# Kernel tuning notes

Measured on AMD Instinct MI355X. Metric: run time of the kernel, lower is better.

The kernel has to match this reference:

```python
import jax, jax.numpy as jnp
import numpy as np

H = 10           # lstm_hidden / attn_hidden
OUT = 2          # output_size
VTH = 0.5        # args.vth (LSNN threshold, beta=0 so fixed)
DT = 1e-3
TAU_SYN_INV = 1.0 / 5e-3
TAU_MEM_INV = 1.0 / 1e-2


def _bn(x, g, b, eps=1e-5):
    # TdBatchNorm1d in ANN mode: BatchNorm1d over channel dim of (B, C, T), batch stats
    m = x.mean(axis=(0, 2), keepdims=True)
    v = x.var(axis=(0, 2), keepdims=True)
    return g[None, :, None] * (x - m) * jax.lax.rsqrt(v + eps) + b[None, :, None]


def _lin(x, W):
    # ModuleLayer(Linear): apply linear over channel dim of (B, C, T)
    return jnp.einsum('bct,hc->bht', x, W)


def setup_inputs() -> dict:
    key = jax.random.key(0)
    ks = jax.random.split(key, 12)
    B, C, T = 32, 64, 1024
    f32 = jnp.float32
    ones = jnp.ones((H,), f32)
    zeros = jnp.zeros((H,), f32)
    def n(k, shape, s=0.3):
        return jax.random.normal(k, shape, f32) * s
    return {
        'bs1': jax.random.normal(ks[0], (B, 1), f32),
        'bs2': jax.random.normal(ks[1], (B, 1), f32),
        'beeg': jax.random.normal(ks[2], (B, C, T), f32),
        'targets': jax.random.randint(ks[3], (B,), 0, 2),
        'W_ef': n(ks[4], (H, C)), 'b_ef': jnp.zeros((H,), f32),
        'g_i': ones, 'be_i': zeros,
        'Wq': n(ks[5], (H, H)), 'g_q': ones, 'be_q': zeros,
        'Wk': n(ks[6], (H, H)), 'g_k': ones, 'be_k': zeros,
        'Wv': n(ks[7], (H, H)), 'g_v': ones, 'be_v': zeros,
        'Wc': n(ks[8], (H, H)), 'g_c': ones, 'be_c': zeros,
        'W_in': n(ks[9], (H, H)), 'W_rec': n(ks[10], (H, H)),
        'W_cls': n(ks[11], (OUT, H)), 'b_cls': jnp.zeros((OUT,), f32),
    }


def _forward(beeg, W_ef, b_ef, g_i, be_i, Wq, g_q, be_q, Wk, g_k, be_k,
             Wv, g_v, be_v, Wc, g_c, be_c, W_in, W_rec, W_cls, b_cls):
    # front embedding + BNi + tanh : (B, C, T) -> (B, H, T)
    x = jnp.tanh(_bn(_lin(beeg, W_ef) + b_ef[None, :, None], g_i, be_i))
    # self-attention (need_sa, full dot_product path)
    q = jax.nn.relu(_bn(_lin(x, Wq), g_q, be_q))
    k = jax.nn.relu(_bn(_lin(x, Wk), g_k, be_k))
    v = jnp.tanh(_bn(_lin(x, Wv), g_v, be_v))
    w = jnp.einsum('bht,bhs->bts', q, k) / H              # (B, T, T)
    av = jnp.einsum('bts,bhs->bht', w, v)                  # (B, H, T)
    x = jax.nn.relu(_bn(_lin(av, Wc), g_c, be_c))
    # LSNN recurrence over time (norse-style LSNN, beta=0, b fixed at VTH)
    xs = jnp.transpose(x, (2, 0, 1))                       # (T, B, H)
    B = xs.shape[1]
    dtype = xs.dtype
    def lsnn_step(state, xt):
        z, vm, cur, b = state
        i_jump = cur + xt @ W_in.T + z @ W_rec.T
        v_dec = vm + DT * TAU_MEM_INV * (i_jump - vm)
        i_dec = i_jump * (1.0 - DT * TAU_SYN_INV)
        z_new = (v_dec > b).astype(dtype)
        v_new = (1.0 - z_new) * v_dec
        return (z_new, v_new, i_dec, b), z_new
    z0 = jnp.zeros((B, H), dtype)
    init = (z0, z0, z0, jnp.full((B, H), VTH, dtype))
    _, zs = jax.lax.scan(lsnn_step, init, xs)              # (T, B, H) spikes
    # LILinearCell classifier, stepped over time, then mean over T
    def li_step(state, zt):
        vm, cur = state
        i_new = cur * (1.0 - DT * TAU_SYN_INV) + zt @ W_cls.T + b_cls
        v_new = vm * (1.0 - DT * TAU_MEM_INV) + DT * TAU_MEM_INV * i_new
        return (v_new, i_new), v_new
    s0 = jnp.zeros((B, OUT), dtype)
    _, vs = jax.lax.scan(li_step, (s0, s0), zs)            # (T, B, 2)
    return vs.mean(axis=0)                                 # (B, 2) = sum/step


def reference(bs1, bs2, beeg, targets, W_ef, b_ef, g_i, be_i, Wq, g_q, be_q,
              Wk, g_k, be_k, Wv, g_v, be_v, Wc, g_c, be_c, W_in, W_rec,
              W_cls, b_cls):
    out = _forward(beeg, W_ef, b_ef, g_i, be_i, Wq, g_q, be_q, Wk, g_k, be_k,
                   Wv, g_v, be_v, Wc, g_c, be_c, W_in, W_rec, W_cls, b_cls)
    return out
```

## Files before the change

### kernel.cpp

```cpp
#include <hip/hip_runtime.h>
#include <math.h>


constexpr int B = 32, C = 64, T = 1024, H = 10;
constexpr int NT = 1024;
constexpr int RS = 1028;

struct Params {
  const float *beeg, *W_ef, *b_ef, *g_i, *be_i, *Wq, *g_q, *be_q, *Wk, *g_k,
      *be_k, *Wv, *g_v, *be_v, *Wc, *g_c, *be_c, *W_in, *W_rec, *W_cls, *b_cls;
  int* cnt;
  double *P1, *P2, *P3;
  float* out;
};

template <int CTRL>
__device__ inline float dadd(float v) {
  int x = __builtin_amdgcn_update_dpp(0, __float_as_int(v), CTRL, 0xf, 0xf,
                                      true);
  return v + __int_as_float(x);
}
__device__ inline float wred63(float v) {
  v = dadd<0x111>(v);
  v = dadd<0x112>(v);
  v = dadd<0x114>(v);
  v = dadd<0x118>(v);
  v = dadd<0x142>(v);
  v = dadd<0x143>(v);
  return v;
}

__device__ inline float ftanh(float x) {
  float e = __builtin_amdgcn_exp2f(x * 2.8853900817779268f);
  float r = __builtin_amdgcn_rcpf(e + 1.0f);
  return fmaf(-2.0f, r, 1.0f);
}

__device__ inline void gbar(int* cnt, int phase, int tid) {
  __syncthreads();
  if (tid == 0) {
    __hip_atomic_fetch_add(&cnt[phase], 1, __ATOMIC_RELEASE,
                           __HIP_MEMORY_SCOPE_AGENT);
    while (__hip_atomic_load(&cnt[phase], __ATOMIC_RELAXED,
                             __HIP_MEMORY_SCOPE_AGENT) < B)
      __builtin_amdgcn_s_sleep(2);
  }
  __syncthreads();
}

__global__ void __launch_bounds__(NT) fused19(Params p) {
  const int b = blockIdx.x, tid = threadIdx.x;
  const int lane = tid & 63, wid = tid >> 6;

  __shared__ __align__(16) float slab[T * 11];
  __shared__ __align__(16) float gtab[T];
  __shared__ double dred2[60 * 17 + 4];
  __shared__ double dtot[60];
  __shared__ float stM[30], stI[30], Ms[100], Nl[100];
  __shared__ float kxl[NT * 11];

  float* swred = slab;
  float* mpw   = slab + 1024;

  {
    const float L2A = -0.15200309344504995f;
    const float L2D = -0.32192809488736235f;
    float m0 = (float)(T - tid);
    gtab[tid] = (9.0f * (1.0f - exp2f(m0 * L2A)) -
                 4.0f * (1.0f - exp2f(m0 * L2D))) * (1.0f / (float)T);
  }

  auto combine = [&](double* P, int Q2) {
    for (int id = tid; id < Q2 * 16; id += NT) {
      int ch = id >> 4, i = id & 15;
      double s = __hip_atomic_load(&P[ch * 32 + i], __ATOMIC_RELAXED,
                                   __HIP_MEMORY_SCOPE_AGENT) +
                 __hip_atomic_load(&P[ch * 32 + 16 + i], __ATOMIC_RELAXED,
                                   __HIP_MEMORY_SCOPE_AGENT);
      dred2[ch * 17 + i] = s;
    }
    __syncthreads();
    if (tid < Q2) {
      double s = 0.0;
#pragma unroll
      for (int i = 0; i < 16; ++i) s += dred2[tid * 17 + i];
      dtot[tid] = s;
    }
    __syncthreads();
  };

  float p1[H];
#pragma unroll
  for (int h = 0; h < H; ++h) p1[h] = p.b_ef[h];
  {
    const float* bp = p.beeg + (size_t)b * C * T;
#pragma unroll 8
    for (int c = 0; c < C; ++c) {
      float v = bp[(size_t)c * T + tid];
#pragma unroll
      for (int h = 0; h < H; ++h)
        p1[h] = fmaf(v, p.W_ef[h * C + c], p1[h]);
    }
  }
#pragma unroll
  for (int h = 0; h < H; ++h) {
    float r1 = wred63(p1[h]);
    float r2 = wred63(p1[h] * p1[h]);
    if (lane == 63) { swred[wid * 60 + h] = r1; swred[wid * 60 + 10 + h] = r2; }
  }
  __syncthreads();
  if (tid < 20) {
    float s = 0.f;
#pragma unroll
    for (int w = 0; w < 16; ++w) s += swred[w * 60 + tid];
    __hip_atomic_store(&p.P1[tid * 32 + b], (double)s, __ATOMIC_RELAXED,
                       __HIP_MEMORY_SCOPE_AGENT);
  }
  gbar(p.cnt, 0, tid);
  combine(p.P1, 20);
  if (tid < 10) {
    double mean = dtot[tid] * (1.0 / 32768.0);
    double var  = dtot[10 + tid] * (1.0 / 32768.0) - mean * mean;
    stM[tid] = (float)mean;
    stI[tid] = (float)(1.0 / sqrt(var + 1e-5));
  }
  __syncthreads();

  float xa[H];
#pragma unroll
  for (int j = 0; j < H; ++j)
    xa[j] = ftanh(p.g_i[j] * (p1[j] - stM[j]) * stI[j] + p.be_i[j]);
#pragma unroll
  for (int h = 0; h < H; ++h) {
    float qa = 0.f, ka = 0.f, va = 0.f;
#pragma unroll
    for (int j = 0; j < H; ++j) {
      qa = fmaf(xa[j], p.Wq[h * H + j], qa);
      ka = fmaf(xa[j], p.Wk[h * H + j], ka);
      va = fmaf(xa[j], p.Wv[h * H + j], va);
    }
    float r1 = wred63(qa), r2 = wred63(qa * qa);
    float r3 = wred63(ka), r4 = wred63(ka * ka);
    float r5 = wred63(va), r6 = wred63(va * va);
    if (lane == 63) {
      swred[wid * 60 + h]      = r1; swred[wid * 60 + 30 + h] = r2;
      swred[wid * 60 + 10 + h] = r3; swred[wid * 60 + 40 + h] = r4;
      swred[wid * 60 + 20 + h] = r5; swred[wid * 60 + 50 + h] = r6;
    }
  }
  __syncthreads();
  if (tid < 60) {
    float s = 0.f;
#pragma unroll
    for (int w = 0; w < 16; ++w) s += swred[w * 60 + tid];
    __hip_atomic_store(&p.P2[tid * 32 + b], (double)s, __ATOMIC_RELAXED,
                       __HIP_MEMORY_SCOPE_AGENT);
  }
  gbar(p.cnt, 1, tid);
  combine(p.P2, 60);
  if (tid < 30) {
    double mean = dtot[tid] * (1.0 / 32768.0);
    double var  = dtot[30 + tid] * (1.0 / 32768.0) - mean * mean;
    stM[tid] = (float)mean;
    stI[tid] = (float)(1.0 / sqrt(var + 1e-5));
  }
  __syncthreads();

  {
    float vx[H];
#pragma unroll
    for (int h = 0; h < H; ++h) {
      float ka = 0.f, va = 0.f;
#pragma unroll
      for (int j = 0; j < H; ++j) {
        ka = fmaf(xa[j], p.Wk[h * H + j], ka);
        va = fmaf(xa[j], p.Wv[h * H + j], va);
      }
      kxl[tid * 11 + h] =
          fmaxf(p.g_k[h] * (ka - stM[10 + h]) * stI[10 + h] + p.be_k[h], 0.f);
      vx[h] = ftanh(p.g_v[h] * (va - stM[20 + h]) * stI[20 + h] + p.be_v[h]);
    }
#pragma unroll 1
    for (int i = 0; i < H; ++i) {
      float ki = kxl[tid * 11 + i];
#pragma unroll
      for (int j = 0; j < H; ++j) {
        float r = wred63(ki * vx[j]);
        if (lane == 63) mpw[wid * 100 + i * 10 + j] = r;
      }
    }
  }
  __syncthreads();
  if (tid < 100) {
    float s = 0.f;
#pragma unroll
    for (int w = 0; w < 16; ++w) s += mpw[w * 100 + tid];
    Ms[tid] = s;
  }
  __syncthreads();

  if (tid < 100) {
    int i = tid / 10, h = tid % 10;
    float a = 0.f;
#pragma unroll
    for (int j = 0; j < H; ++j) a = fmaf(Ms[i * 10 + j], p.Wc[h * H + j], a);
    Nl[tid] = a * 0.1f;
  }
  __syncthreads();
  float pca[H];
  {
    float qv[H];
#pragma unroll
    for (int h = 0; h < H; ++h) {
      float qa = 0.f;
#pragma unroll
      for (int j = 0; j < H; ++j) qa = fmaf(xa[j], p.Wq[h * H + j], qa);
      qv[h] = fmaxf(p.g_q[h] * (qa - stM[h]) * stI[h] + p.be_q[h], 0.f);
    }
#pragma unroll
    for (int h = 0; h < H; ++h) {
      float a = 0.f;
#pragma unroll
      for (int i = 0; i < H; ++i) a = fmaf(qv[i], Nl[i * 10 + h], a);
      pca[h] = a;
    }
  }
#pragma unroll
  for (int h = 0; h < H; ++h) {
    float r1 = wred63(pca[h]);
    float r2 = wred63(pca[h] * pca[h]);
    if (lane == 63) { swred[wid * 60 + h] = r1; swred[wid * 60 + 10 + h] = r2; }
  }
  __syncthreads();
  if (tid < 20) {
    float s = 0.f;
#pragma unroll
    for (int w = 0; w < 16; ++w) s += swred[w * 60 + tid];
    __hip_atomic_store(&p.P3[tid * 32 + b], (double)s, __ATOMIC_RELAXED,
                       __HIP_MEMORY_SCOPE_AGENT);
  }
  gbar(p.cnt, 2, tid);
  combine(p.P3, 20);
  if (tid < 10) {
    double mean = dtot[tid] * (1.0 / 32768.0);
    double var  = dtot[10 + tid] * (1.0 / 32768.0) - mean * mean;
    stM[tid] = (float)mean;
    stI[tid] = (float)(1.0 / sqrt(var + 1e-5));
  }
  __syncthreads();

  {
    float ca[H];
#pragma unroll
    for (int j = 0; j < H; ++j)
      ca[j] = fmaxf(p.g_c[j] * (pca[j] - stM[j]) * stI[j] + p.be_c[j], 0.f);
#pragma unroll
    for (int h = 0; h < H; ++h) {
      float a = 0.f;
#pragma unroll
      for (int j = 0; j < H; ++j) a = fmaf(ca[j], p.W_in[h * H + j], a);
      slab[h * RS + tid] = a;
    }
  }
  __syncthreads();

  if (tid < 64) {
    const float gtot = 4.9365234375f;

    const int slot = lane < H ? lane : 0;
    const float* row = slab + slot * RS;
    float wrf[H];
#pragma unroll
    for (int j = 0; j < H; ++j)
      wrf[j] = (lane < H) ? p.W_rec[lane * H + j] : 0.f;

    float accp = 0.f, vm = 0.f, S = 0.f;
    float zf = 0.f;

    auto step = [&](float iin, float gt) {
      float zj[H];
#pragma unroll
      for (int j = 0; j < H; ++j)
        zj[j] = __int_as_float(
            __builtin_amdgcn_readlane(__float_as_int(zf), j));
      float acc0 = fmaf(0.8f, accp, iin);
      float acc1 = 0.f;
#pragma unroll
      for (int j = 0; j < H; j += 2) {
        acc0 = fmaf(zj[j],     wrf[j],     acc0);
        acc1 = fmaf(zj[j + 1], wrf[j + 1], acc1);
      }
      float acc = acc0 + acc1;
      float v_dec = fmaf(0.1f, acc - vm, vm);
      bool z = v_dec > 0.5f;
      vm = z ? 0.f : v_dec;
      zf = z ? 1.0f : 0.0f;
      S = fmaf(zf, gt, S);
      accp = acc;
    };

    float4 iA = *(const float4*)&row[0];
    float4 iB = *(const float4*)&row[4];
    float4 gA = *(const float4*)&gtab[0], gB = *(const float4*)&gtab[4];

    for (int t8 = 0; t8 < T - 8; t8 += 8) {
      float4 iN1 = *(const float4*)&row[t8 + 8];
      float4 iN2 = *(const float4*)&row[t8 + 12];
      float4 gN1 = *(const float4*)&gtab[t8 + 8];
      float4 gN2 = *(const float4*)&gtab[t8 + 12];
      step(iA.x, gA.x); step(iA.y, gA.y); step(iA.z, gA.z); step(iA.w, gA.w);
      step(iB.x, gB.x); step(iB.y, gB.y); step(iB.z, gB.z); step(iB.w, gB.w);
      iA = iN1; iB = iN2; gA = gN1; gB = gN2;
    }
    step(iA.x, gA.x); step(iA.y, gA.y); step(iA.z, gA.z); step(iA.w, gA.w);
    step(iB.x, gB.x); step(iB.y, gB.y); step(iB.z, gB.z); step(iB.w, gB.w);

    int li = lane < H ? lane : 0;
    float c0 = (lane < H) ? S * p.W_cls[li]     : 0.f;
    float c1 = (lane < H) ? S * p.W_cls[H + li] : 0.f;
    float r0 = wred63(c0), r1 = wred63(c1);
    if (lane == 63) {
      p.out[b * 2 + 0] = r0 + gtot * p.b_cls[0];
      p.out[b * 2 + 1] = r1 + gtot * p.b_cls[1];
    }
  }
}

extern "C" void kernel_launch(void* const* d_in, const int* in_sizes, int n_in,
                              void* d_out, int out_size, void* d_ws, size_t ws_size,
                              hipStream_t stream) {
  Params p;
  p.beeg  = (const float*)d_in[2];
  p.W_ef  = (const float*)d_in[4];
  p.b_ef  = (const float*)d_in[5];
  p.g_i   = (const float*)d_in[6];
  p.be_i  = (const float*)d_in[7];
  p.Wq    = (const float*)d_in[8];
  p.g_q   = (const float*)d_in[9];
  p.be_q  = (const float*)d_in[10];
  p.Wk    = (const float*)d_in[11];
  p.g_k   = (const float*)d_in[12];
  p.be_k  = (const float*)d_in[13];
  p.Wv    = (const float*)d_in[14];
  p.g_v   = (const float*)d_in[15];
  p.be_v  = (const float*)d_in[16];
  p.Wc    = (const float*)d_in[17];
  p.g_c   = (const float*)d_in[18];
  p.be_c  = (const float*)d_in[19];
  p.W_in  = (const float*)d_in[20];
  p.W_rec = (const float*)d_in[21];
  p.W_cls = (const float*)d_in[22];
  p.b_cls = (const float*)d_in[23];

  char* ws = (char*)d_ws;
  p.cnt = (int*)ws;
  p.P1  = (double*)(ws + 256);
  p.P2  = (double*)(ws + 256 + 5120);
  p.P3  = (double*)(ws + 256 + 5120 + 15360);
  p.out = (float*)d_out;

  (void)hipMemsetAsync(d_ws, 0, 256, stream);
  fused19<<<dim3(B), dim3(NT), 0, stream>>>(p);
}
```

Baseline: 221.9 us.

## Halve block size and process two timesteps per thread with packed FMA

Reduces the block from 1024 to 512 threads, with each thread handling timesteps t and t+512. The per-thread math uses two-wide float vectors so the compiler can emit packed FMA instructions. The two halves are summed before each wave reduction, so cross-wave reduction work halves. The kxl scratch buffer is dropped in favour of a transposed layout reusing the slab, which needs an extra barrier. The costs are more registers per thread and less thread-level parallelism during the serial-heavy phases.

```diff
diff --git a/kernel.cpp b/kernel.cpp
--- a/kernel.cpp
+++ b/kernel.cpp
@@ -3,8 +3,14 @@
 
 
 constexpr int B = 32, C = 64, T = 1024, H = 10;
-constexpr int NT = 1024;
+constexpr int NT = 512;
 constexpr int RS = 1028;
+
+using v2f = float __attribute__((ext_vector_type(2)));
+__device__ inline v2f v2(float s) { v2f r; r.x = s; r.y = s; return r; }
+__device__ inline v2f vfma(v2f a, v2f b, v2f c) {
+  return __builtin_elementwise_fma(a, b, c);
+}
 
 struct Params {
   const float *beeg, *W_ef, *b_ef, *g_i, *be_i, *Wq, *g_q, *be_q, *Wk, *g_k,
@@ -48,26 +54,29 @@
   __syncthreads();
 }
 
-__global__ void __launch_bounds__(NT) fused19(Params p) {
+__global__ void __launch_bounds__(NT) fused21(Params p) {
   const int b = blockIdx.x, tid = threadIdx.x;
   const int lane = tid & 63, wid = tid >> 6;
+  const int t0 = tid, t1 = tid + NT;
 
   __shared__ __align__(16) float slab[T * 11];
   __shared__ __align__(16) float gtab[T];
   __shared__ double dred2[60 * 17 + 4];
   __shared__ double dtot[60];
   __shared__ float stM[30], stI[30], Ms[100], Nl[100];
-  __shared__ float kxl[NT * 11];
 
   float* swred = slab;
-  float* mpw   = slab + 1024;
+  float* kxt   = slab;
+  float* mpw   = slab + 10240;
 
   {
     const float L2A = -0.15200309344504995f;
     const float L2D = -0.32192809488736235f;
-    float m0 = (float)(T - tid);
-    gtab[tid] = (9.0f * (1.0f - exp2f(m0 * L2A)) -
-                 4.0f * (1.0f - exp2f(m0 * L2D))) * (1.0f / (float)T);
+    float m0 = (float)(T - t0), m1 = (float)(T - t1);
+    gtab[t0] = (9.0f * (1.0f - exp2f(m0 * L2A)) -
+                4.0f * (1.0f - exp2f(m0 * L2D))) * (1.0f / (float)T);
+    gtab[t1] = (9.0f * (1.0f - exp2f(m1 * L2A)) -
+                4.0f * (1.0f - exp2f(m1 * L2D))) * (1.0f / (float)T);
   }
 
   auto combine = [&](double* P, int Q2) {
@@ -89,30 +98,32 @@
     __syncthreads();
   };
 
-  float p1[H];
-#pragma unroll
-  for (int h = 0; h < H; ++h) p1[h] = p.b_ef[h];
+  v2f p1[H];
+#pragma unroll
+  for (int h = 0; h < H; ++h) p1[h] = v2(p.b_ef[h]);
   {
     const float* bp = p.beeg + (size_t)b * C * T;
 #pragma unroll 8
     for (int c = 0; c < C; ++c) {
-      float v = bp[(size_t)c * T + tid];
+      v2f vab;
+      vab.x = bp[(size_t)c * T + t0];
+      vab.y = bp[(size_t)c * T + t1];
 #pragma unroll
       for (int h = 0; h < H; ++h)
-        p1[h] = fmaf(v, p.W_ef[h * C + c], p1[h]);
+        p1[h] = vfma(vab, v2(p.W_ef[h * C + c]), p1[h]);
     }
   }
 #pragma unroll
   for (int h = 0; h < H; ++h) {
-    float r1 = wred63(p1[h]);
-    float r2 = wred63(p1[h] * p1[h]);
+    float r1 = wred63(p1[h].x + p1[h].y);
+    float r2 = wred63(p1[h].x * p1[h].x + p1[h].y * p1[h].y);
     if (lane == 63) { swred[wid * 60 + h] = r1; swred[wid * 60 + 10 + h] = r2; }
   }
   __syncthreads();
   if (tid < 20) {
     float s = 0.f;
 #pragma unroll
-    for (int w = 0; w < 16; ++w) s += swred[w * 60 + tid];
+    for (int w = 0; w < 8; ++w) s += swred[w * 60 + tid];
     __hip_atomic_store(&p.P1[tid * 32 + b], (double)s, __ATOMIC_RELAXED,
                        __HIP_MEMORY_SCOPE_AGENT);
   }
@@ -126,22 +137,24 @@
   }
   __syncthreads();
 
-  float xa[H];
-#pragma unroll
-  for (int j = 0; j < H; ++j)
-    xa[j] = ftanh(p.g_i[j] * (p1[j] - stM[j]) * stI[j] + p.be_i[j]);
+  v2f xv[H];
+#pragma unroll
+  for (int j = 0; j < H; ++j) {
+    xv[j].x = ftanh(p.g_i[j] * (p1[j].x - stM[j]) * stI[j] + p.be_i[j]);
+    xv[j].y = ftanh(p.g_i[j] * (p1[j].y - stM[j]) * stI[j] + p.be_i[j]);
+  }
 #pragma unroll
   for (int h = 0; h < H; ++h) {
-    float qa = 0.f, ka = 0.f, va = 0.f;
+    v2f q = v2(0.f), k = v2(0.f), v = v2(0.f);
 #pragma unroll
     for (int j = 0; j < H; ++j) {
-      qa = fmaf(xa[j], p.Wq[h * H + j], qa);
-      ka = fmaf(xa[j], p.Wk[h * H + j], ka);
-      va = fmaf(xa[j], p.Wv[h * H + j], va);
-    }
-    float r1 = wred63(qa), r2 = wred63(qa * qa);
-    float r3 = wred63(ka), r4 = wred63(ka * ka);
-    float r5 = wred63(va), r6 = wred63(va * va);
+      q = vfma(xv[j], v2(p.Wq[h * H + j]), q);
+      k = vfma(xv[j], v2(p.Wk[h * H + j]), k);
+      v = vfma(xv[j], v2(p.Wv[h * H + j]), v);
+    }
+    float r1 = wred63(q.x + q.y), r2 = wred63(q.x * q.x + q.y * q.y);
+    float r3 = wred63(k.x + k.y), r4 = wred63(k.x * k.x + k.y * k.y);
+    float r5 = wred63(v.x + v.y), r6 = wred63(v.x * v.x + v.y * v.y);
     if (lane == 63) {
       swred[wid * 60 + h]      = r1; swred[wid * 60 + 30 + h] = r2;
       swred[wid * 60 + 10 + h] = r3; swred[wid * 60 + 40 + h] = r4;
@@ -152,7 +165,7 @@
   if (tid < 60) {
     float s = 0.f;
 #pragma unroll
-    for (int w = 0; w < 16; ++w) s += swred[w * 60 + tid];
+    for (int w = 0; w < 8; ++w) s += swred[w * 60 + tid];
     __hip_atomic_store(&p.P2[tid * 32 + b], (double)s, __ATOMIC_RELAXED,
                        __HIP_MEMORY_SCOPE_AGENT);
   }
@@ -167,25 +180,30 @@
   __syncthreads();
 
   {
-    float vx[H];
+    v2f vx[H];
 #pragma unroll
     for (int h = 0; h < H; ++h) {
-      float ka = 0.f, va = 0.f;
+      v2f k = v2(0.f), v = v2(0.f);
 #pragma unroll
       for (int j = 0; j < H; ++j) {
-        ka = fmaf(xa[j], p.Wk[h * H + j], ka);
-        va = fmaf(xa[j], p.Wv[h * H + j], va);
+        k = vfma(xv[j], v2(p.Wk[h * H + j]), k);
+        v = vfma(xv[j], v2(p.Wv[h * H + j]), v);
       }
-      kxl[tid * 11 + h] =
-          fmaxf(p.g_k[h] * (ka - stM[10 + h]) * stI[10 + h] + p.be_k[h], 0.f);
-      vx[h] = ftanh(p.g_v[h] * (va - stM[20 + h]) * stI[20 + h] + p.be_v[h]);
-    }
+      kxt[h * NT + tid] =
+          fmaxf(p.g_k[h] * (k.x - stM[10 + h]) * stI[10 + h] + p.be_k[h], 0.f);
+      kxt[(H + h) * NT + tid] =
+          fmaxf(p.g_k[h] * (k.y - stM[10 + h]) * stI[10 + h] + p.be_k[h], 0.f);
+      vx[h].x = ftanh(p.g_v[h] * (v.x - stM[20 + h]) * stI[20 + h] + p.be_v[h]);
+      vx[h].y = ftanh(p.g_v[h] * (v.y - stM[20 + h]) * stI[20 + h] + p.be_v[h]);
+    }
+    __syncthreads();
 #pragma unroll 1
     for (int i = 0; i < H; ++i) {
-      float ki = kxl[tid * 11 + i];
+      float kia = kxt[i * NT + tid];
+      float kib = kxt[(H + i) * NT + tid];
 #pragma unroll
       for (int j = 0; j < H; ++j) {
-        float r = wred63(ki * vx[j]);
+        float r = wred63(fmaf(kia, vx[j].x, kib * vx[j].y));
         if (lane == 63) mpw[wid * 100 + i * 10 + j] = r;
       }
     }
@@ -194,7 +212,7 @@
   if (tid < 100) {
     float s = 0.f;
 #pragma unroll
-    for (int w = 0; w < 16; ++w) s += mpw[w * 100 + tid];
+    for (int w = 0; w < 8; ++w) s += mpw[w * 100 + tid];
     Ms[tid] = s;
   }
   __syncthreads();
@@ -207,35 +225,36 @@
     Nl[tid] = a * 0.1f;
   }
   __syncthreads();
-  float pca[H];
-  {
-    float qv[H];
+  v2f pc[H];
+  {
+    v2f qv[H];
 #pragma unroll
     for (int h = 0; h < H; ++h) {
-      float qa = 0.f;
-#pragma unroll
-      for (int j = 0; j < H; ++j) qa = fmaf(xa[j], p.Wq[h * H + j], qa);
-      qv[h] = fmaxf(p.g_q[h] * (qa - stM[h]) * stI[h] + p.be_q[h], 0.f);
+      v2f qa = v2(0.f);
+#pragma unroll
+      for (int j = 0; j < H; ++j) qa = vfma(xv[j], v2(p.Wq[h * H + j]), qa);
+      qv[h].x = fmaxf(p.g_q[h] * (qa.x - stM[h]) * stI[h] + p.be_q[h], 0.f);
+      qv[h].y = fmaxf(p.g_q[h] * (qa.y - stM[h]) * stI[h] + p.be_q[h], 0.f);
     }
 #pragma unroll
     for (int h = 0; h < H; ++h) {
-      float a = 0.f;
-#pragma unroll
-      for (int i = 0; i < H; ++i) a = fmaf(qv[i], Nl[i * 10 + h], a);
-      pca[h] = a;
+      v2f a = v2(0.f);
+#pragma unroll
+      for (int i = 0; i < H; ++i) a = vfma(qv[i], v2(Nl[i * 10 + h]), a);
+      pc[h] = a;
     }
   }
 #pragma unroll
   for (int h = 0; h < H; ++h) {
-    float r1 = wred63(pca[h]);
-    float r2 = wred63(pca[h] * pca[h]);
+    float r1 = wred63(pc[h].x + pc[h].y);
+    float r2 = wred63(pc[h].x * pc[h].x + pc[h].y * pc[h].y);
     if (lane == 63) { swred[wid * 60 + h] = r1; swred[wid * 60 + 10 + h] = r2; }
   }
   __syncthreads();
   if (tid < 20) {
     float s = 0.f;
 #pragma unroll
-    for (int w = 0; w < 16; ++w) s += swred[w * 60 + tid];
+    for (int w = 0; w < 8; ++w) s += swred[w * 60 + tid];
     __hip_atomic_store(&p.P3[tid * 32 + b], (double)s, __ATOMIC_RELAXED,
                        __HIP_MEMORY_SCOPE_AGENT);
   }
@@ -250,16 +269,19 @@
   __syncthreads();
 
   {
-    float ca[H];
-#pragma unroll
-    for (int j = 0; j < H; ++j)
-      ca[j] = fmaxf(p.g_c[j] * (pca[j] - stM[j]) * stI[j] + p.be_c[j], 0.f);
+    v2f ca[H];
+#pragma unroll
+    for (int j = 0; j < H; ++j) {
+      ca[j].x = fmaxf(p.g_c[j] * (pc[j].x - stM[j]) * stI[j] + p.be_c[j], 0.f);
+      ca[j].y = fmaxf(p.g_c[j] * (pc[j].y - stM[j]) * stI[j] + p.be_c[j], 0.f);
+    }
 #pragma unroll
     for (int h = 0; h < H; ++h) {
-      float a = 0.f;
-#pragma unroll
-      for (int j = 0; j < H; ++j) a = fmaf(ca[j], p.W_in[h * H + j], a);
-      slab[h * RS + tid] = a;
+      v2f a = v2(0.f);
+#pragma unroll
+      for (int j = 0; j < H; ++j) a = vfma(ca[j], v2(p.W_in[h * H + j]), a);
+      slab[h * RS + t0] = a.x;
+      slab[h * RS + t1] = a.y;
     }
   }
   __syncthreads();
@@ -360,5 +382,5 @@
   p.out = (float*)d_out;
 
   (void)hipMemsetAsync(d_ws, 0, 256, stream);
-  fused19<<<dim3(B), dim3(NT), 0, stream>>>(p);
-}
+  fused21<<<dim3(B), dim3(NT), 0, stream>>>(p);
+}
```

New measurement: 198.8 us. -10.4%, faster.
